# Optimization experiments

Hardware: AMD Instinct MI355X
Metric: run time of the kernel (lower is better)

The kernel has to match this reference:

```python
import jax, jax.numpy as jnp
import numpy as np

E, H = 1024, 16


def setup_inputs() -> dict:
    key = jax.random.key(0)
    k1, k2, k3, k4 = jax.random.split(key, 4)
    B, L = 4, 2048
    embeddings = jax.random.normal(k1, (B, L, E), dtype=jnp.float32)
    mask = jax.random.randint(k2, (B, L, L), 0, 2) == 1  # True = masked out
    # Params (torch Linear y = x @ W.T; we store already-transposed [in, out])
    W_qkv = jax.random.normal(k3, (E, 3 * E), dtype=jnp.float32) * 0.02
    W_out = jax.random.normal(k4, (E, E), dtype=jnp.float32) * 0.02
    return {"embeddings": embeddings, "mask": mask, "W_qkv": W_qkv, "W_out": W_out}


def reference(embeddings, mask, W_qkv, W_out):
    B, L, E_ = embeddings.shape
    A = E_ // H
    scale = A ** (-0.5)
    qkv = embeddings @ W_qkv                       # [B, L, 3E]
    qkv = qkv.reshape(B, L, H, 3 * A).transpose(0, 2, 1, 3)  # [B, H, L, 3A]
    q, k, v = jnp.split(qkv, 3, axis=-1)           # each [B, H, L, A]
    scores = jnp.einsum('bhqa,bhka->bhqk', q, k) * scale  # [B, H, L, L]
    m = mask[:, None, :, :]                        # [B, 1, L, L]
    fully = jnp.all(m, axis=-1, keepdims=True)     # rows with every key masked
    scores = jnp.where(m, -jnp.inf, scores)
    scores = jnp.where(fully, 0.0, scores)         # keep softmax finite
    attn = jax.nn.softmax(scores, axis=-1)
    attn = jnp.where(fully, 0.0, attn)             # == torch nan_to_num(0)
    values = jnp.einsum('bhqk,bhka->bhqa', attn, v)  # [B, H, L, A]
    values = values.transpose(0, 2, 1, 3).reshape(B, L, E_)
    return values @ W_out
```

## Files before the change

### kernel.cpp

```cpp
#include <hip/hip_runtime.h>
#include <hip/hip_bf16.h>

#define B_   4
#define L_   2048
#define E_   1024
#define H_   16
#define T_   8192
#define K_   1024

typedef __attribute__((ext_vector_type(8))) short bf16x8;
typedef __attribute__((ext_vector_type(4))) float f32x4;

__device__ __forceinline__ ushort f2b(float f) {
    union { float f; unsigned u; } x; x.f = f;
    unsigned r = (x.u + 0x7fffu + ((x.u >> 16) & 1u)) >> 16;
    return (ushort)r;
}

#define GLD_LDS16(gp, lp) __builtin_amdgcn_global_load_lds( \
    (const __attribute__((address_space(1))) void*)(gp), \
    (__attribute__((address_space(3))) void*)(lp), 16, 0, 0)

__global__ void detect_mask_layout(const unsigned char* __restrict__ m, int* flag) {
    __shared__ int s;
    if (threadIdx.x == 0) s = 0;
    __syncthreads();
    int found = 0;
    for (int i = threadIdx.x; i < 4096; i += 256)
        if ((i & 3) != 0 && m[i] != 0) found = 1;
    if (found) atomicOr(&s, 1);
    __syncthreads();
    if (threadIdx.x == 0) *flag = s;
}

__global__ void pack_mask(const void* __restrict__ mraw, const int* __restrict__ flag,
                          unsigned long long* __restrict__ bits) {
    int row  = blockIdx.x;
    int lane = threadIdx.x & 63;
    int wave = threadIdx.x >> 6;
    int isByte = *flag;
    const unsigned char* mb = (const unsigned char*)mraw;
    const int*           mi = (const int*)mraw;
    long long base = (long long)row * L_;
    for (int w = wave; w < 32; w += 4) {
        int idx = w * 64 + lane;
        int v = isByte ? (int)mb[base + idx] : mi[base + idx];
        unsigned long long word = __ballot(v == 0);
        if (lane == 0) bits[row * 32 + w] = word;
    }
}

__global__ __launch_bounds__(256) void conv_bf16(const float* __restrict__ in,
                                                 ushort* __restrict__ out) {
    int i = blockIdx.x * 256 + threadIdx.x;
    float4 v = ((const float4*)in)[i];
    ushort4 o;
    o.x = f2b(v.x); o.y = f2b(v.y); o.z = f2b(v.z); o.w = f2b(v.w);
    ((ushort4*)out)[i] = o;
}

__global__ __launch_bounds__(256) void transpose_conv(const float* __restrict__ in,
        ushort* __restrict__ out, int R, int Cn) {
    __shared__ float t[32][33];
    int c0 = blockIdx.x * 32, r0 = blockIdx.y * 32;
    int x = threadIdx.x & 31, y = threadIdx.x >> 5;
#pragma unroll
    for (int k = 0; k < 4; ++k)
        t[y + k * 8][x] = in[(size_t)(r0 + y + k * 8) * Cn + c0 + x];
    __syncthreads();
#pragma unroll
    for (int k = 0; k < 4; ++k)
        out[(size_t)(c0 + y + k * 8) * R + r0 + x] = f2b(t[x][y + k * 8]);
}

template<int NDIM, int MODE>
__global__ __launch_bounds__(256) void gemm_bf16(
        const ushort* __restrict__ Ab, const ushort* __restrict__ Bt,
        float* __restrict__ Cg, ushort* __restrict__ Qb,
        ushort* __restrict__ Kb, ushort* __restrict__ Vt) {
    __shared__ ushort As[128 * 64];
    __shared__ ushort Bs[128 * 64];
    const int tid = threadIdx.x;
    const int wv = tid >> 6, ln = tid & 63;
    const int bn = blockIdx.x * 128, bm = blockIdx.y * 128;
    const int wm = (wv & 1) * 64, wn = (wv >> 1) * 64;
    const int row16 = ln & 15, quad = ln >> 4;
    const int cg8 = (((ln & 7) ^ (ln >> 3)) * 8);

    f32x4 acc[4][4];
#pragma unroll
    for (int i = 0; i < 4; ++i)
#pragma unroll
        for (int j = 0; j < 4; ++j) acc[i][j] = (f32x4){0.f, 0.f, 0.f, 0.f};

    for (int k0 = 0; k0 < K_; k0 += 64) {
        __syncthreads();
#pragma unroll
        for (int it = 0; it < 4; ++it) {
            int rA = wv * 32 + it * 8 + (ln >> 3);
            GLD_LDS16(Ab + (size_t)(bm + rA) * K_ + k0 + cg8, &As[(wv * 32 + it * 8) * 64]);
            GLD_LDS16(Bt + (size_t)(bn + rA) * K_ + k0 + cg8, &Bs[(wv * 32 + it * 8) * 64]);
        }
        __syncthreads();
#pragma unroll
        for (int ks = 0; ks < 2; ++ks) {
            const int ch = (((ks * 4 + quad) ^ (ln & 7)) * 8);
            bf16x8 af[4], bf[4];
#pragma unroll
            for (int i = 0; i < 4; ++i)
                af[i] = *(const bf16x8*)&As[(wm + i * 16 + row16) * 64 + ch];
#pragma unroll
            for (int j = 0; j < 4; ++j)
                bf[j] = *(const bf16x8*)&Bs[(wn + j * 16 + row16) * 64 + ch];
#pragma unroll
            for (int i = 0; i < 4; ++i)
#pragma unroll
                for (int j = 0; j < 4; ++j)
                    acc[i][j] = __builtin_amdgcn_mfma_f32_16x16x32_bf16(
                        af[i], bf[j], acc[i][j], 0, 0, 0);
        }
    }

    if (MODE == 0) {
#pragma unroll
        for (int i = 0; i < 4; ++i)
#pragma unroll
            for (int j = 0; j < 4; ++j) {
                int col = bn + wn + j * 16 + row16;
#pragma unroll
                for (int r = 0; r < 4; ++r) {
                    int row = bm + wm + i * 16 + quad * 4 + r;
                    Cg[(size_t)row * NDIM + col] = acc[i][j][r];
                }
            }
    } else {
#pragma unroll
        for (int j = 0; j < 4; ++j) {
            int col = bn + wn + j * 16 + row16;
            int h = col / 192, w = col - h * 192;
            int sel = w >> 6, a = w & 63;
#pragma unroll
            for (int i = 0; i < 4; ++i)
#pragma unroll
                for (int r = 0; r < 4; ++r) {
                    int rowg = bm + wm + i * 16 + quad * 4 + r;
                    int b = rowg >> 11, l = rowg & 2047;
                    ushort v = f2b(acc[i][j][r]);
                    size_t bh = (size_t)(b * H_ + h);
                    if (sel == 0)      Qb[(bh * L_ + l) * 64 + a] = v;
                    else if (sel == 1) Kb[(bh * L_ + l) * 64 + a] = v;
                    else               Vt[(bh * 64 + a) * L_ + l] = v;
                }
        }
    }
}

__global__ __launch_bounds__(256) void attn_mfma(
        const ushort* __restrict__ Qb, const ushort* __restrict__ Kb,
        const ushort* __restrict__ Vt, const unsigned long long* __restrict__ bits,
        ushort* __restrict__ vals) {
    __shared__ ushort Qs[64 * 64];
    __shared__ ushort Ks[64 * 64];
    __shared__ ushort Vs[64 * 64];
    __shared__ ushort Ps[4][16 * 64];

    const int tid = threadIdx.x, wv = tid >> 6, ln = tid & 63;
    const int bh = blockIdx.y, b = bh >> 4, h = bh & 15;
    const int q0 = blockIdx.x * 64;
    const int row16 = ln & 15, quad = ln >> 4;
    const int cg8 = (((ln & 7) ^ (ln >> 3)) * 8);
    const float CSC = 0.125f * 1.44269504f;

    {
        const ushort* Qg = Qb + ((size_t)bh * L_ + q0) * 64;
#pragma unroll
        for (int it = 0; it < 2; ++it) {
            int r = wv * 16 + it * 8 + (ln >> 3);
            GLD_LDS16(Qg + (size_t)r * 64 + cg8, &Qs[(wv * 16 + it * 8) * 64]);
        }
    }
    __syncthreads();

    const int ch0 = ((quad ^ (ln & 7)) * 8);
    const int ch1 = (((4 + quad) ^ (ln & 7)) * 8);
    bf16x8 aq[2];
    aq[0] = *(const bf16x8*)&Qs[(wv * 16 + row16) * 64 + ch0];
    aq[1] = *(const bf16x8*)&Qs[(wv * 16 + row16) * 64 + ch1];

    bf16x8 vone;
#pragma unroll
    for (int i = 0; i < 8; ++i) vone[i] = (short)0x3F80;

    f32x4 oacc[4], lacc;
#pragma unroll
    for (int t = 0; t < 4; ++t) oacc[t] = (f32x4){0.f, 0.f, 0.f, 0.f};
    lacc = (f32x4){0.f, 0.f, 0.f, 0.f};

    const unsigned long long* bp[4];
#pragma unroll
    for (int r = 0; r < 4; ++r)
        bp[r] = bits + ((size_t)b * L_ + q0 + wv * 16 + quad * 4 + r) * 32;

    const ushort* Kg = Kb + (size_t)bh * L_ * 64;
    const ushort* Vg = Vt + (size_t)bh * 64 * L_;
    const int rh = row16 >> 3, rl = row16 & 7;
    const int pw = ((quad * 4) & 7);

    for (int kt = 0; kt < 32; ++kt) {
        __syncthreads();
#pragma unroll
        for (int it = 0; it < 2; ++it) {
            int r = wv * 16 + it * 8 + (ln >> 3);
            GLD_LDS16(Kg + (size_t)(kt * 64 + r) * 64 + cg8, &Ks[(wv * 16 + it * 8) * 64]);
            GLD_LDS16(Vg + (size_t)r * L_ + kt * 64 + cg8,   &Vs[(wv * 16 + it * 8) * 64]);
        }
        __syncthreads();

        f32x4 sa[4];
#pragma unroll
        for (int t = 0; t < 4; ++t) sa[t] = (f32x4){0.f, 0.f, 0.f, 0.f};
#pragma unroll
        for (int t = 0; t < 4; ++t) {
            bf16x8 bk0 = *(const bf16x8*)&Ks[(t * 16 + row16) * 64 + ch0];
            sa[t] = __builtin_amdgcn_mfma_f32_16x16x32_bf16(aq[0], bk0, sa[t], 0, 0, 0);
            bf16x8 bk1 = *(const bf16x8*)&Ks[(t * 16 + row16) * 64 + ch1];
            sa[t] = __builtin_amdgcn_mfma_f32_16x16x32_bf16(aq[1], bk1, sa[t], 0, 0, 0);
        }

#pragma unroll
        for (int r = 0; r < 4; ++r) {
            unsigned long long sh = bp[r][kt] >> row16;
            unsigned lo = (unsigned)sh, hi = (unsigned)(sh >> 32);
            float p0 = (lo & 1u)       ? exp2f(sa[0][r] * CSC) : 0.f;
            float p1 = (lo & 0x10000u) ? exp2f(sa[1][r] * CSC) : 0.f;
            float p2 = (hi & 1u)       ? exp2f(sa[2][r] * CSC) : 0.f;
            float p3 = (hi & 0x10000u) ? exp2f(sa[3][r] * CSC) : 0.f;
            ushort* pr = &Ps[wv][(quad * 4 + r) * 64];
            int px = (pw + r) & 7;
            pr[((0 + rh) ^ px) * 8 + rl] = f2b(p0);
            pr[((2 + rh) ^ px) * 8 + rl] = f2b(p1);
            pr[((4 + rh) ^ px) * 8 + rl] = f2b(p2);
            pr[((6 + rh) ^ px) * 8 + rl] = f2b(p3);
        }

        {
            bf16x8 ap0 = *(const bf16x8*)&Ps[wv][row16 * 64 + ch0];
            lacc = __builtin_amdgcn_mfma_f32_16x16x32_bf16(ap0, vone, lacc, 0, 0, 0);
#pragma unroll
            for (int t = 0; t < 4; ++t) {
                bf16x8 bv = *(const bf16x8*)&Vs[(t * 16 + row16) * 64 + ch0];
                oacc[t] = __builtin_amdgcn_mfma_f32_16x16x32_bf16(ap0, bv, oacc[t], 0, 0, 0);
            }
            bf16x8 ap1 = *(const bf16x8*)&Ps[wv][row16 * 64 + ch1];
            lacc = __builtin_amdgcn_mfma_f32_16x16x32_bf16(ap1, vone, lacc, 0, 0, 0);
#pragma unroll
            for (int t = 0; t < 4; ++t) {
                bf16x8 bv = *(const bf16x8*)&Vs[(t * 16 + row16) * 64 + ch1];
                oacc[t] = __builtin_amdgcn_mfma_f32_16x16x32_bf16(ap1, bv, oacc[t], 0, 0, 0);
            }
        }
    }

#pragma unroll
    for (int r = 0; r < 4; ++r) {
        float l = lacc[r];
        float inv = (l > 0.f) ? 1.0f / l : 0.f;
        int qrow = q0 + wv * 16 + quad * 4 + r;
        size_t base = ((size_t)b * L_ + qrow) * E_ + h * 64;
#pragma unroll
        for (int t = 0; t < 4; ++t)
            vals[base + t * 16 + row16] = f2b(oacc[t][r] * inv);
    }
}

extern "C" void kernel_launch(void* const* d_in, const int* in_sizes, int n_in,
                              void* d_out, int out_size, void* d_ws, size_t ws_size,
                              hipStream_t stream) {
    const float* emb  = (const float*)d_in[0];
    const void*  mask = d_in[1];
    const float* wqkv = (const float*)d_in[2];
    const float* wout = (const float*)d_in[3];
    float* out = (float*)d_out;

    char* ws = (char*)d_ws;
    const size_t NEED = 4096ull + 2097152ull + 2ull * 46137344ull;
    if (ws_size < NEED) return;

    int* flag = (int*)ws;
    unsigned long long* bits = (unsigned long long*)(ws + 4096);
    ushort* embb  = (ushort*)(ws + 4096 + 2097152);
    ushort* Wqkvt = embb  + 8388608;
    ushort* Wott  = Wqkvt + 3145728;
    ushort* Qb    = Wott  + 1048576;
    ushort* Kb    = Qb    + 8388608;
    ushort* Vt    = Kb    + 8388608;
    ushort* vals  = Vt    + 8388608;

    detect_mask_layout<<<1, 256, 0, stream>>>((const unsigned char*)mask, flag);
    pack_mask<<<T_, 256, 0, stream>>>(mask, flag, bits);
    conv_bf16<<<8192, 256, 0, stream>>>(emb, embb);
    transpose_conv<<<dim3(96, 32), 256, 0, stream>>>(wqkv, Wqkvt, 1024, 3072);
    transpose_conv<<<dim3(32, 32), 256, 0, stream>>>(wout, Wott, 1024, 1024);
    gemm_bf16<3072, 1><<<dim3(24, 64), 256, 0, stream>>>(
        embb, Wqkvt, nullptr, Qb, Kb, Vt);
    attn_mfma<<<dim3(32, 64), 256, 0, stream>>>(Qb, Kb, Vt, bits, vals);
    gemm_bf16<1024, 0><<<dim3(8, 64), 256, 0, stream>>>(
        vals, Wott, out, nullptr, nullptr, nullptr);
}
```

Measured before the change: 437.7 us.

## Fold softmax scale into Q, pack bf16 conversions, reuse Q LDS for P

Moves the softmax scale times log2(e) into the QKV GEMM epilogue, so Q is stored pre-scaled and the attention loop computes exp2 without a multiply. Mask-word loads are issued before the barrier so they overlap the K/V tile fetch. Exponentials are converted with a packed bf16 instruction and masked with bit operations instead of branches. The Q staging buffer is reused for the per-wave P tiles to shrink LDS. Exp2 is now computed for masked entries too, and Q rounding to bf16 happens after scaling, which slightly changes numerics.

```diff
diff --git a/kernel.cpp b/kernel.cpp
--- a/kernel.cpp
+++ b/kernel.cpp
@@ -11,10 +11,21 @@
 typedef __attribute__((ext_vector_type(8))) short bf16x8;
 typedef __attribute__((ext_vector_type(4))) float f32x4;
 
+#define CSC_ (0.125f * 1.44269504f)
+
 __device__ __forceinline__ ushort f2b(float f) {
     union { float f; unsigned u; } x; x.f = f;
     unsigned r = (x.u + 0x7fffu + ((x.u >> 16) & 1u)) >> 16;
     return (ushort)r;
+}
+
+__device__ __forceinline__ unsigned pack2bf(float a, float b) {
+#if __has_builtin(__builtin_amdgcn_cvt_pk_bf16_f32)
+    auto t = __builtin_amdgcn_cvt_pk_bf16_f32(a, b);
+    return __builtin_bit_cast(unsigned, t);
+#else
+    return (unsigned)f2b(a) | ((unsigned)f2b(b) << 16);
+#endif
 }
 
 #define GLD_LDS16(gp, lp) __builtin_amdgcn_global_load_lds( \
@@ -54,9 +65,10 @@
                                                  ushort* __restrict__ out) {
     int i = blockIdx.x * 256 + threadIdx.x;
     float4 v = ((const float4*)in)[i];
-    ushort4 o;
-    o.x = f2b(v.x); o.y = f2b(v.y); o.z = f2b(v.z); o.w = f2b(v.w);
-    ((ushort4*)out)[i] = o;
+    uint2 o;
+    o.x = pack2bf(v.x, v.y);
+    o.y = pack2bf(v.z, v.w);
+    ((uint2*)out)[i] = o;
 }
 
 __global__ __launch_bounds__(256) void transpose_conv(const float* __restrict__ in,
@@ -139,13 +151,14 @@
             int col = bn + wn + j * 16 + row16;
             int h = col / 192, w = col - h * 192;
             int sel = w >> 6, a = w & 63;
+            float qs = (sel == 0) ? CSC_ : 1.0f;
 #pragma unroll
             for (int i = 0; i < 4; ++i)
 #pragma unroll
                 for (int r = 0; r < 4; ++r) {
                     int rowg = bm + wm + i * 16 + quad * 4 + r;
                     int b = rowg >> 11, l = rowg & 2047;
-                    ushort v = f2b(acc[i][j][r]);
+                    ushort v = f2b(acc[i][j][r] * qs);
                     size_t bh = (size_t)(b * H_ + h);
                     if (sel == 0)      Qb[(bh * L_ + l) * 64 + a] = v;
                     else if (sel == 1) Kb[(bh * L_ + l) * 64 + a] = v;
@@ -159,24 +172,22 @@
         const ushort* __restrict__ Qb, const ushort* __restrict__ Kb,
         const ushort* __restrict__ Vt, const unsigned long long* __restrict__ bits,
         ushort* __restrict__ vals) {
-    __shared__ ushort Qs[64 * 64];
     __shared__ ushort Ks[64 * 64];
     __shared__ ushort Vs[64 * 64];
-    __shared__ ushort Ps[4][16 * 64];
+    __shared__ ushort PQ[64 * 64];
 
     const int tid = threadIdx.x, wv = tid >> 6, ln = tid & 63;
     const int bh = blockIdx.y, b = bh >> 4, h = bh & 15;
     const int q0 = blockIdx.x * 64;
     const int row16 = ln & 15, quad = ln >> 4;
     const int cg8 = (((ln & 7) ^ (ln >> 3)) * 8);
-    const float CSC = 0.125f * 1.44269504f;
 
     {
         const ushort* Qg = Qb + ((size_t)bh * L_ + q0) * 64;
 #pragma unroll
         for (int it = 0; it < 2; ++it) {
-            int r = wv * 16 + it * 8 + (ln >> 3);
-            GLD_LDS16(Qg + (size_t)r * 64 + cg8, &Qs[(wv * 16 + it * 8) * 64]);
+            GLD_LDS16(Qg + (size_t)(wv * 16 + it * 8 + (ln >> 3)) * 64 + cg8,
+                      &PQ[(wv * 16 + it * 8) * 64]);
         }
     }
     __syncthreads();
@@ -184,8 +195,9 @@
     const int ch0 = ((quad ^ (ln & 7)) * 8);
     const int ch1 = (((4 + quad) ^ (ln & 7)) * 8);
     bf16x8 aq[2];
-    aq[0] = *(const bf16x8*)&Qs[(wv * 16 + row16) * 64 + ch0];
-    aq[1] = *(const bf16x8*)&Qs[(wv * 16 + row16) * 64 + ch1];
+    aq[0] = *(const bf16x8*)&PQ[(wv * 16 + row16) * 64 + ch0];
+    aq[1] = *(const bf16x8*)&PQ[(wv * 16 + row16) * 64 + ch1];
+    ushort* Pw = &PQ[wv * 1024];
 
     bf16x8 vone;
 #pragma unroll
@@ -196,15 +208,13 @@
     for (int t = 0; t < 4; ++t) oacc[t] = (f32x4){0.f, 0.f, 0.f, 0.f};
     lacc = (f32x4){0.f, 0.f, 0.f, 0.f};
 
-    const unsigned long long* bp[4];
-#pragma unroll
-    for (int r = 0; r < 4; ++r)
-        bp[r] = bits + ((size_t)b * L_ + q0 + wv * 16 + quad * 4 + r) * 32;
+    const unsigned long long* bpp =
+        bits + ((size_t)b * L_ + q0 + wv * 16 + quad * 4) * 32;
 
     const ushort* Kg = Kb + (size_t)bh * L_ * 64;
     const ushort* Vg = Vt + (size_t)bh * 64 * L_;
     const int rh = row16 >> 3, rl = row16 & 7;
-    const int pw = ((quad * 4) & 7);
+    const int pxb = (quad * 4) & 7;
 
     for (int kt = 0; kt < 32; ++kt) {
         __syncthreads();
@@ -214,6 +224,8 @@
             GLD_LDS16(Kg + (size_t)(kt * 64 + r) * 64 + cg8, &Ks[(wv * 16 + it * 8) * 64]);
             GLD_LDS16(Vg + (size_t)r * L_ + kt * 64 + cg8,   &Vs[(wv * 16 + it * 8) * 64]);
         }
+        unsigned long long wm0 = bpp[kt], wm1 = bpp[kt + 32],
+                           wm2 = bpp[kt + 64], wm3 = bpp[kt + 96];
         __syncthreads();
 
         f32x4 sa[4];
@@ -227,31 +239,32 @@
             sa[t] = __builtin_amdgcn_mfma_f32_16x16x32_bf16(aq[1], bk1, sa[t], 0, 0, 0);
         }
 
+        unsigned long long wmv[4] = {wm0, wm1, wm2, wm3};
 #pragma unroll
         for (int r = 0; r < 4; ++r) {
-            unsigned long long sh = bp[r][kt] >> row16;
+            unsigned long long sh = wmv[r] >> row16;
             unsigned lo = (unsigned)sh, hi = (unsigned)(sh >> 32);
-            float p0 = (lo & 1u)       ? exp2f(sa[0][r] * CSC) : 0.f;
-            float p1 = (lo & 0x10000u) ? exp2f(sa[1][r] * CSC) : 0.f;
-            float p2 = (hi & 1u)       ? exp2f(sa[2][r] * CSC) : 0.f;
-            float p3 = (hi & 0x10000u) ? exp2f(sa[3][r] * CSC) : 0.f;
-            ushort* pr = &Ps[wv][(quad * 4 + r) * 64];
-            int px = (pw + r) & 7;
-            pr[((0 + rh) ^ px) * 8 + rl] = f2b(p0);
-            pr[((2 + rh) ^ px) * 8 + rl] = f2b(p1);
-            pr[((4 + rh) ^ px) * 8 + rl] = f2b(p2);
-            pr[((6 + rh) ^ px) * 8 + rl] = f2b(p3);
+            unsigned pk01 = pack2bf(exp2f(sa[0][r]), exp2f(sa[1][r]));
+            unsigned pk23 = pack2bf(exp2f(sa[2][r]), exp2f(sa[3][r]));
+            pk01 &= (lo & 0x00010001u) * 0xFFFFu;
+            pk23 &= (hi & 0x00010001u) * 0xFFFFu;
+            ushort* pr = Pw + (quad * 4 + r) * 64;
+            int px = pxb + r;
+            pr[((0 + rh) ^ px) * 8 + rl] = (ushort)pk01;
+            pr[((2 + rh) ^ px) * 8 + rl] = (ushort)(pk01 >> 16);
+            pr[((4 + rh) ^ px) * 8 + rl] = (ushort)pk23;
+            pr[((6 + rh) ^ px) * 8 + rl] = (ushort)(pk23 >> 16);
         }
 
         {
-            bf16x8 ap0 = *(const bf16x8*)&Ps[wv][row16 * 64 + ch0];
+            bf16x8 ap0 = *(const bf16x8*)&Pw[row16 * 64 + ch0];
             lacc = __builtin_amdgcn_mfma_f32_16x16x32_bf16(ap0, vone, lacc, 0, 0, 0);
 #pragma unroll
             for (int t = 0; t < 4; ++t) {
                 bf16x8 bv = *(const bf16x8*)&Vs[(t * 16 + row16) * 64 + ch0];
                 oacc[t] = __builtin_amdgcn_mfma_f32_16x16x32_bf16(ap0, bv, oacc[t], 0, 0, 0);
             }
-            bf16x8 ap1 = *(const bf16x8*)&Ps[wv][row16 * 64 + ch1];
+            bf16x8 ap1 = *(const bf16x8*)&Pw[row16 * 64 + ch1];
             lacc = __builtin_amdgcn_mfma_f32_16x16x32_bf16(ap1, vone, lacc, 0, 0, 0);
 #pragma unroll
             for (int t = 0; t < 4; ++t) {
```

Result: faster. 425.1 us (-2.9%).
